# Performance work log

Hardware: AMD Instinct MI355X
Metric: run time of the kernel (lower is better)

Reference implementation:

```python
import jax, jax.numpy as jnp
import numpy as np

DIM = 2048
MLP_MULT = 4
NUM_EXPERTS = 8
EXPERT_INTER = MLP_MULT * DIM // NUM_EXPERTS  # 1024
B, S = 4, 2048


def setup_inputs() -> dict:
    key = jax.random.key(0)
    k1, k2, k3, k4 = jax.random.split(key, 4)
    x = jax.random.normal(k1, (B, S, DIM), dtype=jnp.float32)
    expert_ids = jax.random.randint(k2, (B, S), 0, NUM_EXPERTS, dtype=jnp.int64)
    # kaiming-uniform-ish scale for gate_up; down_proj random (zeros in orig init
    # would make output trivially zero, unhelpful for a correctness baseline)
    bound_gu = float(np.sqrt(1.0 / DIM))
    gate_up_proj = jax.random.uniform(k3, (NUM_EXPERTS, DIM, 2 * EXPERT_INTER),
                                      dtype=jnp.float32, minval=-bound_gu, maxval=bound_gu)
    bound_dn = float(np.sqrt(1.0 / EXPERT_INTER))
    down_proj = jax.random.uniform(k4, (NUM_EXPERTS, EXPERT_INTER, DIM),
                                   dtype=jnp.float32, minval=-bound_dn, maxval=bound_dn)
    return {"x": x, "expert_ids": expert_ids,
            "gate_up_proj": gate_up_proj, "down_proj": down_proj}


def reference(x, expert_ids, gate_up_proj, down_proj):
    Bb, Ss, D = x.shape
    E = gate_up_proj.shape[0]
    flat_x = x.reshape(-1, D)            # [T, D], T = B*S
    flat_ids = expert_ids.reshape(-1)    # [T]
    # Same math as the torch loop: full dense per-expert MLP, then mask.
    gu = jnp.einsum('td,edh->eth', flat_x, gate_up_proj)       # [E, T, 2I]
    g, u = jnp.split(gu, 2, axis=-1)                           # [E, T, I] each
    h = jax.nn.silu(g) * u                                     # [E, T, I]
    y = jnp.einsum('eti,eid->etd', h, down_proj)               # [E, T, D]
    mask = (flat_ids[None, :] == jnp.arange(E)[:, None])[..., None]  # [E, T, 1]
    out = jnp.sum(y * mask.astype(y.dtype), axis=0)            # [T, D]
    return out.reshape(Bb, Ss, D)
```

## Files before the change

kernel.cpp:

```cpp
#include <hip/hip_runtime.h>
#include <cstdint>
#include <cstddef>


typedef __attribute__((ext_vector_type(8))) _Float16 half8;
typedef __attribute__((ext_vector_type(4))) float floatx4;

#define AS_G __attribute__((address_space(1)))
#define AS_L __attribute__((address_space(3)))

__device__ __forceinline__ void async_cp16(void* lds, const void* g) {
  __builtin_amdgcn_global_load_lds((const AS_G uint32_t*)g, (AS_L uint32_t*)lds,
                                   16, 0, 0);
}

static constexpr int TTOK = 8192;
static constexpr int DIMK = 2048;
static constexpr int EI = 1024;
static constexpr int NE = 8;
static constexpr int PADT = 9216;
static constexpr int MAXTILES = 80;
static constexpr int NTILE_LAUNCH = 72;

__global__ __launch_bounds__(256) void k_route(const int* __restrict__ ids,
                                               int* __restrict__ perm,
                                               int* __restrict__ te,
                                               int* __restrict__ tr0,
                                               int* __restrict__ tnr,
                                               int* __restrict__ cur) {
  __shared__ int cnt[NE];
  __shared__ int sstart[NE];
  __shared__ int snpad[NE];
  __shared__ int stotal;
  int tid = threadIdx.x;
  if (tid < NE) cnt[tid] = 0;
  __syncthreads();
  for (int t = tid; t < TTOK; t += 256) atomicAdd(&cnt[ids[t]], 1);
  __syncthreads();
  if (tid == 0) {
    int pr = 0, nt = 0;
    for (int e = 0; e < NE; e++) {
      int n = cnt[e];
      sstart[e] = pr;
      cur[e] = pr;
      int padded = ((n + 127) >> 7) << 7;
      snpad[e] = padded - n;
      for (int j = 0; j < n; j += 128) {
        te[nt] = e; tr0[nt] = pr + j; tnr[nt] = min(128, n - j); nt++;
      }
      pr += padded;
    }
    stotal = pr;
    for (; nt < MAXTILES; nt++) { te[nt] = 0; tr0[nt] = 0; tnr[nt] = 0; }
  }
  __syncthreads();
  for (int e = 0; e < NE; e++) {
    int base = sstart[e] + cnt[e];
    for (int i = tid; i < snpad[e]; i += 256) perm[base + i] = 0;
  }
  for (int i = stotal + tid; i < PADT; i += 256) perm[i] = 0;
}

__global__ __launch_bounds__(256) void k_scatter(const int* __restrict__ ids,
                                                 int* __restrict__ cur,
                                                 int* __restrict__ perm) {
  __shared__ int bcnt[NE], bbase[NE], bloc[NE];
  int tid = threadIdx.x;
  int t = blockIdx.x * 256 + tid;
  if (tid < NE) { bcnt[tid] = 0; bloc[tid] = 0; }
  __syncthreads();
  int e = ids[t];
  atomicAdd(&bcnt[e], 1);
  __syncthreads();
  if (tid < NE && bcnt[tid] > 0) bbase[tid] = atomicAdd(&cur[tid], bcnt[tid]);
  __syncthreads();
  int off = atomicAdd(&bloc[e], 1);
  perm[bbase[e] + off] = t;
}

template <int K, int N>
__device__ __forceinline__ void transpose_tile(const float* __restrict__ src,
                                               _Float16* __restrict__ dst,
                                               float (*tile)[67], int e,
                                               int n0, int k0, int tid) {
  const float* s = src + (size_t)e * K * N;
  _Float16* d = dst + (size_t)e * N * K;
  int kk = tid >> 4;
  int nn = (tid & 15) * 4;
#pragma unroll
  for (int i = 0; i < 4; i++) {
    float4 v = *(const float4*)(s + (size_t)(k0 + kk + i * 16) * N + n0 + nn);
    tile[kk + i * 16][nn + 0] = v.x;
    tile[kk + i * 16][nn + 1] = v.y;
    tile[kk + i * 16][nn + 2] = v.z;
    tile[kk + i * 16][nn + 3] = v.w;
  }
  __syncthreads();
  int nrow = tid >> 3;
  int k8 = (tid & 7) * 8;
#pragma unroll
  for (int i = 0; i < 2; i++) {
    int n = nrow + i * 32;
    half8 o;
#pragma unroll
    for (int j = 0; j < 8; j++) o[j] = (_Float16)tile[k8 + j][n];
    *(half8*)(d + (size_t)(n0 + n) * K + k0 + k8) = o;
  }
}

__global__ __launch_bounds__(256) void k_prep(const float* __restrict__ gup,
                                              _Float16* __restrict__ wt1,
                                              const float* __restrict__ x,
                                              const int* __restrict__ perm,
                                              _Float16* __restrict__ xg) {
  __shared__ float tile[64][67];
  int b = blockIdx.x;
  int tid = threadIdx.x;
  if (b < 8192) {
    int e = b >> 10;
    int r = b & 1023;
    transpose_tile<DIMK, DIMK>(gup, wt1, tile, e, (r & 31) * 64, (r >> 5) * 64,
                               tid);
  } else {
    int row = b - 8192;
    int tok = perm[row];
    int c = tid * 8;
    const float* s = x + (size_t)tok * DIMK + c;
    float4 a = *(const float4*)s;
    float4 bb = *(const float4*)(s + 4);
    half8 o;
    o[0] = (_Float16)a.x; o[1] = (_Float16)a.y;
    o[2] = (_Float16)a.z; o[3] = (_Float16)a.w;
    o[4] = (_Float16)bb.x; o[5] = (_Float16)bb.y;
    o[6] = (_Float16)bb.z; o[7] = (_Float16)bb.w;
    *(half8*)(xg + (size_t)row * DIMK + c) = o;
  }
}

__global__ __launch_bounds__(256) void k_t2(const float* __restrict__ dwn,
                                            _Float16* __restrict__ wt2) {
  __shared__ float tile[64][67];
  transpose_tile<EI, DIMK>(dwn, wt2, tile, blockIdx.z, blockIdx.x * 64,
                           blockIdx.y * 64, threadIdx.x);
}

__global__ __launch_bounds__(256) void k_gateup(
    const _Float16* __restrict__ xg, const _Float16* __restrict__ wt1,
    const int* __restrict__ te, const int* __restrict__ tr0,
    const int* __restrict__ tnr, _Float16* __restrict__ hbuf) {
  int flat = blockIdx.y * 16 + blockIdx.x;
  int swz = (flat & 7) * (NTILE_LAUNCH * 16 / 8) + (flat >> 3);
  int tile = swz >> 4;
  int nr = tnr[tile];
  if (nr == 0) return;
  int e = te[tile], r0 = tr0[tile];
  int col = (swz & 15) * 64;
  int tid = threadIdx.x;

  __shared__ __align__(16) _Float16 As[2][128 * 64];
  __shared__ __align__(16) _Float16 Bg[2][64 * 64];
  __shared__ __align__(16) _Float16 Bu[2][64 * 64];

  int an = tid >> 2;
  int aq = (tid & 3) ^ ((tid >> 3) & 3);
  const _Float16* ap0 = xg + (size_t)(r0 + an) * DIMK + aq * 8;
  const _Float16* ap1 = ap0 + (size_t)64 * DIMK;
  const _Float16* bgp =
      wt1 + (size_t)e * DIMK * DIMK + (size_t)(col + an) * DIMK + aq * 8;
  const _Float16* bup = bgp + (size_t)EI * DIMK;

  int wave = tid >> 6, lane = tid & 63;
  int wm = (wave & 1) * 64, wn = (wave >> 1) * 32;
  int lm = lane & 15, lq = lane >> 4;
  int aoff[4], boff[2];
#pragma unroll
  for (int i = 0; i < 4; i++) {
    int r = wm + i * 16 + lm;
    aoff[i] = (r * 4 + (lq ^ ((r >> 1) & 3))) * 8;
  }
#pragma unroll
  for (int j = 0; j < 2; j++) {
    int n = wn + j * 16 + lm;
    boff[j] = (n * 4 + (lq ^ ((n >> 1) & 3))) * 8;
  }

  floatx4 accg[4][2], accu[4][2];
#pragma unroll
  for (int i = 0; i < 4; i++)
#pragma unroll
    for (int j = 0; j < 2; j++) {
      accg[i][j] = (floatx4)0.0f;
      accu[i][j] = (floatx4)0.0f;
    }

  auto stage = [&](int p, int k0) {
    _Float16* a = As[p] + (size_t)tid * 8;
    _Float16* g = Bg[p] + (size_t)tid * 8;
    _Float16* u = Bu[p] + (size_t)tid * 8;
    async_cp16(a, ap0 + k0);
    async_cp16(a + 2048, ap1 + k0);
    async_cp16(g, bgp + k0);
    async_cp16(u, bup + k0);
    async_cp16(a + 4096, ap0 + k0 + 32);
    async_cp16(a + 6144, ap1 + k0 + 32);
    async_cp16(g + 2048, bgp + k0 + 32);
    async_cp16(u + 2048, bup + k0 + 32);
  };

  stage(0, 0);
  __syncthreads();

  int p = 0;
  for (int k0 = 0; k0 < DIMK; k0 += 64, p ^= 1) {
    if (k0 + 64 < DIMK) stage(p ^ 1, k0 + 64);
#pragma unroll
    for (int s = 0; s < 2; s++) {
      const _Float16* Ab = As[p] + s * 4096;
      const _Float16* Bgb = Bg[p] + s * 2048;
      const _Float16* Bub = Bu[p] + s * 2048;
      half8 af[4], bgf[2], buf_[2];
#pragma unroll
      for (int i = 0; i < 4; i++) af[i] = *(const half8*)(Ab + aoff[i]);
#pragma unroll
      for (int j = 0; j < 2; j++) {
        bgf[j] = *(const half8*)(Bgb + boff[j]);
        buf_[j] = *(const half8*)(Bub + boff[j]);
      }
#pragma unroll
      for (int i = 0; i < 4; i++)
#pragma unroll
        for (int j = 0; j < 2; j++) {
          accg[i][j] = __builtin_amdgcn_mfma_f32_16x16x32_f16(
              af[i], bgf[j], accg[i][j], 0, 0, 0);
          accu[i][j] = __builtin_amdgcn_mfma_f32_16x16x32_f16(
              af[i], buf_[j], accu[i][j], 0, 0, 0);
        }
    }
    __syncthreads();
  }

#pragma unroll
  for (int i = 0; i < 4; i++) {
    int rbase = wm + i * 16 + lq * 4;
#pragma unroll
    for (int j = 0; j < 2; j++) {
      int c = col + wn + j * 16 + lm;
#pragma unroll
      for (int rr = 0; rr < 4; rr++) {
        float g = accg[i][j][rr];
        float u = accu[i][j][rr];
        float h = g / (1.0f + __expf(-g)) * u;
        hbuf[(size_t)(r0 + rbase + rr) * EI + c] = (_Float16)h;
      }
    }
  }
}

__global__ __launch_bounds__(256) void k_down(
    const _Float16* __restrict__ hbuf, const _Float16* __restrict__ wt2,
    const int* __restrict__ perm, const int* __restrict__ te,
    const int* __restrict__ tr0, const int* __restrict__ tnr,
    float* __restrict__ out) {
  int flat = blockIdx.y * 16 + blockIdx.x;
  int swz = (flat & 7) * (NTILE_LAUNCH * 16 / 8) + (flat >> 3);
  int tile = swz >> 4;
  int nr = tnr[tile];
  if (nr == 0) return;
  int e = te[tile], r0 = tr0[tile];
  int col = (swz & 15) * 128;
  int tid = threadIdx.x;

  __shared__ __align__(16) _Float16 As[2][128 * 64];
  __shared__ __align__(16) _Float16 Bs[2][128 * 64];

  int an = tid >> 2;
  int aq = (tid & 3) ^ ((tid >> 3) & 3);
  const _Float16* ap0 = hbuf + (size_t)(r0 + an) * EI + aq * 8;
  const _Float16* ap1 = ap0 + (size_t)64 * EI;
  const _Float16* wte = wt2 + (size_t)e * DIMK * EI;
  const _Float16* bp0 = wte + (size_t)(col + an) * EI + aq * 8;
  const _Float16* bp1 = bp0 + (size_t)64 * EI;

  int wave = tid >> 6, lane = tid & 63;
  int wm = (wave & 1) * 64, wn = (wave >> 1) * 64;
  int lm = lane & 15, lq = lane >> 4;
  int aoff[4], boff[4];
#pragma unroll
  for (int i = 0; i < 4; i++) {
    int r = wm + i * 16 + lm;
    aoff[i] = (r * 4 + (lq ^ ((r >> 1) & 3))) * 8;
    int n = wn + i * 16 + lm;
    boff[i] = (n * 4 + (lq ^ ((n >> 1) & 3))) * 8;
  }

  floatx4 acc[4][4];
#pragma unroll
  for (int i = 0; i < 4; i++)
#pragma unroll
    for (int j = 0; j < 4; j++) acc[i][j] = (floatx4)0.0f;

  auto stage = [&](int p, int k0) {
    _Float16* a = As[p] + (size_t)tid * 8;
    _Float16* b = Bs[p] + (size_t)tid * 8;
    async_cp16(a, ap0 + k0);
    async_cp16(a + 2048, ap1 + k0);
    async_cp16(b, bp0 + k0);
    async_cp16(b + 2048, bp1 + k0);
    async_cp16(a + 4096, ap0 + k0 + 32);
    async_cp16(a + 6144, ap1 + k0 + 32);
    async_cp16(b + 4096, bp0 + k0 + 32);
    async_cp16(b + 6144, bp1 + k0 + 32);
  };

  stage(0, 0);
  __syncthreads();

  int p = 0;
  for (int k0 = 0; k0 < EI; k0 += 64, p ^= 1) {
    if (k0 + 64 < EI) stage(p ^ 1, k0 + 64);
#pragma unroll
    for (int s = 0; s < 2; s++) {
      const _Float16* Ab = As[p] + s * 4096;
      const _Float16* Bb = Bs[p] + s * 4096;
      half8 af[4], bf[4];
#pragma unroll
      for (int i = 0; i < 4; i++) {
        af[i] = *(const half8*)(Ab + aoff[i]);
        bf[i] = *(const half8*)(Bb + boff[i]);
      }
#pragma unroll
      for (int i = 0; i < 4; i++)
#pragma unroll
        for (int j = 0; j < 4; j++)
          acc[i][j] = __builtin_amdgcn_mfma_f32_16x16x32_f16(af[i], bf[j],
                                                             acc[i][j], 0, 0, 0);
    }
    __syncthreads();
  }

#pragma unroll
  for (int i = 0; i < 4; i++) {
    int rbase = wm + i * 16 + lq * 4;
#pragma unroll
    for (int rr = 0; rr < 4; rr++) {
      int r = rbase + rr;
      if (r < nr) {
        int tok = perm[r0 + r];
        float* orow = out + (size_t)tok * DIMK + col;
#pragma unroll
        for (int j = 0; j < 4; j++) orow[wn + j * 16 + lm] = acc[i][j][rr];
      }
    }
  }
}

extern "C" void kernel_launch(void* const* d_in, const int* in_sizes, int n_in,
                              void* d_out, int out_size, void* d_ws,
                              size_t ws_size, hipStream_t stream) {
  const float* x = (const float*)d_in[0];
  const int* ids = (const int*)d_in[1];
  const float* gup = (const float*)d_in[2];
  const float* dwn = (const float*)d_in[3];
  float* out = (float*)d_out;
  char* ws = (char*)d_ws;

  int* perm = (int*)ws;
  int* te = (int*)(ws + 36864);
  int* tr0 = (int*)(ws + 36864 + 512);
  int* tnr = (int*)(ws + 36864 + 1024);
  int* cur = (int*)(ws + 36864 + 1536);
  _Float16* wt1 = (_Float16*)(ws + 65536);
  _Float16* hbuf = (_Float16*)(ws + 65536 + 67108864);
  _Float16* xg = (_Float16*)(ws + 65536 + 67108864 + 18874368);
  _Float16* wt2 = wt1;

  k_route<<<dim3(1), dim3(256), 0, stream>>>(ids, perm, te, tr0, tnr, cur);
  k_scatter<<<dim3(32), dim3(256), 0, stream>>>(ids, cur, perm);
  k_prep<<<dim3(8192 + PADT), dim3(256), 0, stream>>>(gup, wt1, x, perm, xg);
  k_gateup<<<dim3(16, NTILE_LAUNCH), dim3(256), 0, stream>>>(
      xg, wt1, te, tr0, tnr, hbuf);
  k_t2<<<dim3(32, 16, 8), dim3(256), 0, stream>>>(dwn, wt2);
  k_down<<<dim3(16, NTILE_LAUNCH), dim3(256), 0, stream>>>(
      hbuf, wt2, perm, te, tr0, tnr, out);
}
```

Before: 500.1 us.

## Deepen GEMM pipelines to four-stage K32 ring with vmcnt-based waits

Both grouped GEMM kernels switch from a double-buffered K=64 loop with __syncthreads to a four-buffer ring of K=32 slices. Three stages stay in flight, and each step waits only for the oldest slice with explicit s_waitcnt vmcnt and a bare s_barrier. MFMA blocks are wrapped in sched_barrier and s_setprio to raise wave priority during matrix math. The intent is to hide global-load latency better and cut the cost of the full sync. In exchange there is one barrier per 32-wide K step instead of per 64. Correctness now depends on hand-tuned vmcnt counts.

```diff
diff --git a/kernel.cpp b/kernel.cpp
--- a/kernel.cpp
+++ b/kernel.cpp
@@ -157,9 +157,9 @@
   int col = (swz & 15) * 64;
   int tid = threadIdx.x;
 
-  __shared__ __align__(16) _Float16 As[2][128 * 64];
-  __shared__ __align__(16) _Float16 Bg[2][64 * 64];
-  __shared__ __align__(16) _Float16 Bu[2][64 * 64];
+  __shared__ __align__(16) _Float16 As[4][4096];
+  __shared__ __align__(16) _Float16 Bg[4][2048];
+  __shared__ __align__(16) _Float16 Bu[4][2048];
 
   int an = tid >> 2;
   int aq = (tid & 3) ^ ((tid >> 3) & 3);
@@ -194,50 +194,59 @@
     }
 
   auto stage = [&](int p, int k0) {
-    _Float16* a = As[p] + (size_t)tid * 8;
-    _Float16* g = Bg[p] + (size_t)tid * 8;
-    _Float16* u = Bu[p] + (size_t)tid * 8;
-    async_cp16(a, ap0 + k0);
-    async_cp16(a + 2048, ap1 + k0);
-    async_cp16(g, bgp + k0);
-    async_cp16(u, bup + k0);
-    async_cp16(a + 4096, ap0 + k0 + 32);
-    async_cp16(a + 6144, ap1 + k0 + 32);
-    async_cp16(g + 2048, bgp + k0 + 32);
-    async_cp16(u + 2048, bup + k0 + 32);
+    async_cp16(&As[p][(size_t)tid * 8], ap0 + k0);
+    async_cp16(&As[p][2048 + (size_t)tid * 8], ap1 + k0);
+    async_cp16(&Bg[p][(size_t)tid * 8], bgp + k0);
+    async_cp16(&Bu[p][(size_t)tid * 8], bup + k0);
   };
 
+  auto compute = [&](int b) {
+    half8 af[4], bgf[2], buf_[2];
+#pragma unroll
+    for (int i = 0; i < 4; i++) af[i] = *(const half8*)(&As[b][0] + aoff[i]);
+#pragma unroll
+    for (int j = 0; j < 2; j++) {
+      bgf[j] = *(const half8*)(&Bg[b][0] + boff[j]);
+      buf_[j] = *(const half8*)(&Bu[b][0] + boff[j]);
+    }
+    asm volatile("s_waitcnt lgkmcnt(0)" ::: "memory");
+    __builtin_amdgcn_sched_barrier(0);
+    __builtin_amdgcn_s_setprio(1);
+#pragma unroll
+    for (int i = 0; i < 4; i++)
+#pragma unroll
+      for (int j = 0; j < 2; j++) {
+        accg[i][j] = __builtin_amdgcn_mfma_f32_16x16x32_f16(
+            af[i], bgf[j], accg[i][j], 0, 0, 0);
+        accu[i][j] = __builtin_amdgcn_mfma_f32_16x16x32_f16(
+            af[i], buf_[j], accu[i][j], 0, 0, 0);
+      }
+    __builtin_amdgcn_s_setprio(0);
+  };
+
   stage(0, 0);
-  __syncthreads();
-
-  int p = 0;
-  for (int k0 = 0; k0 < DIMK; k0 += 64, p ^= 1) {
-    if (k0 + 64 < DIMK) stage(p ^ 1, k0 + 64);
-#pragma unroll
-    for (int s = 0; s < 2; s++) {
-      const _Float16* Ab = As[p] + s * 4096;
-      const _Float16* Bgb = Bg[p] + s * 2048;
-      const _Float16* Bub = Bu[p] + s * 2048;
-      half8 af[4], bgf[2], buf_[2];
-#pragma unroll
-      for (int i = 0; i < 4; i++) af[i] = *(const half8*)(Ab + aoff[i]);
-#pragma unroll
-      for (int j = 0; j < 2; j++) {
-        bgf[j] = *(const half8*)(Bgb + boff[j]);
-        buf_[j] = *(const half8*)(Bub + boff[j]);
-      }
-#pragma unroll
-      for (int i = 0; i < 4; i++)
-#pragma unroll
-        for (int j = 0; j < 2; j++) {
-          accg[i][j] = __builtin_amdgcn_mfma_f32_16x16x32_f16(
-              af[i], bgf[j], accg[i][j], 0, 0, 0);
-          accu[i][j] = __builtin_amdgcn_mfma_f32_16x16x32_f16(
-              af[i], buf_[j], accu[i][j], 0, 0, 0);
-        }
-    }
-    __syncthreads();
-  }
+  stage(1, 32);
+  stage(2, 64);
+
+  int b = 0;
+  for (int k = 0; k < 61; ++k) {
+    asm volatile("s_waitcnt vmcnt(8)" ::: "memory");
+    __builtin_amdgcn_s_barrier();
+    stage((b + 3) & 3, (k + 3) * 32);
+    compute(b);
+    b = (b + 1) & 3;
+  }
+  asm volatile("s_waitcnt vmcnt(8)" ::: "memory");
+  __builtin_amdgcn_s_barrier();
+  compute(b);
+  b = (b + 1) & 3;
+  asm volatile("s_waitcnt vmcnt(4)" ::: "memory");
+  __builtin_amdgcn_s_barrier();
+  compute(b);
+  b = (b + 1) & 3;
+  asm volatile("s_waitcnt vmcnt(0)" ::: "memory");
+  __builtin_amdgcn_s_barrier();
+  compute(b);
 
 #pragma unroll
   for (int i = 0; i < 4; i++) {
@@ -270,8 +279,8 @@
   int col = (swz & 15) * 128;
   int tid = threadIdx.x;
 
-  __shared__ __align__(16) _Float16 As[2][128 * 64];
-  __shared__ __align__(16) _Float16 Bs[2][128 * 64];
+  __shared__ __align__(16) _Float16 As[4][4096];
+  __shared__ __align__(16) _Float16 Bs[4][4096];
 
   int an = tid >> 2;
   int aq = (tid & 3) ^ ((tid >> 3) & 3);
@@ -300,43 +309,54 @@
     for (int j = 0; j < 4; j++) acc[i][j] = (floatx4)0.0f;
 
   auto stage = [&](int p, int k0) {
-    _Float16* a = As[p] + (size_t)tid * 8;
-    _Float16* b = Bs[p] + (size_t)tid * 8;
-    async_cp16(a, ap0 + k0);
-    async_cp16(a + 2048, ap1 + k0);
-    async_cp16(b, bp0 + k0);
-    async_cp16(b + 2048, bp1 + k0);
-    async_cp16(a + 4096, ap0 + k0 + 32);
-    async_cp16(a + 6144, ap1 + k0 + 32);
-    async_cp16(b + 4096, bp0 + k0 + 32);
-    async_cp16(b + 6144, bp1 + k0 + 32);
+    async_cp16(&As[p][(size_t)tid * 8], ap0 + k0);
+    async_cp16(&As[p][2048 + (size_t)tid * 8], ap1 + k0);
+    async_cp16(&Bs[p][(size_t)tid * 8], bp0 + k0);
+    async_cp16(&Bs[p][2048 + (size_t)tid * 8], bp1 + k0);
   };
 
+  auto compute = [&](int b) {
+    half8 af[4], bf[4];
+#pragma unroll
+    for (int i = 0; i < 4; i++) {
+      af[i] = *(const half8*)(&As[b][0] + aoff[i]);
+      bf[i] = *(const half8*)(&Bs[b][0] + boff[i]);
+    }
+    asm volatile("s_waitcnt lgkmcnt(0)" ::: "memory");
+    __builtin_amdgcn_sched_barrier(0);
+    __builtin_amdgcn_s_setprio(1);
+#pragma unroll
+    for (int i = 0; i < 4; i++)
+#pragma unroll
+      for (int j = 0; j < 4; j++)
+        acc[i][j] = __builtin_amdgcn_mfma_f32_16x16x32_f16(af[i], bf[j],
+                                                           acc[i][j], 0, 0, 0);
+    __builtin_amdgcn_s_setprio(0);
+  };
+
   stage(0, 0);
-  __syncthreads();
-
-  int p = 0;
-  for (int k0 = 0; k0 < EI; k0 += 64, p ^= 1) {
-    if (k0 + 64 < EI) stage(p ^ 1, k0 + 64);
-#pragma unroll
-    for (int s = 0; s < 2; s++) {
-      const _Float16* Ab = As[p] + s * 4096;
-      const _Float16* Bb = Bs[p] + s * 4096;
-      half8 af[4], bf[4];
-#pragma unroll
-      for (int i = 0; i < 4; i++) {
-        af[i] = *(const half8*)(Ab + aoff[i]);
-        bf[i] = *(const half8*)(Bb + boff[i]);
-      }
-#pragma unroll
-      for (int i = 0; i < 4; i++)
-#pragma unroll
-        for (int j = 0; j < 4; j++)
-          acc[i][j] = __builtin_amdgcn_mfma_f32_16x16x32_f16(af[i], bf[j],
-                                                             acc[i][j], 0, 0, 0);
-    }
-    __syncthreads();
-  }
+  stage(1, 32);
+  stage(2, 64);
+
+  int b = 0;
+  for (int k = 0; k < 29; ++k) {
+    asm volatile("s_waitcnt vmcnt(8)" ::: "memory");
+    __builtin_amdgcn_s_barrier();
+    stage((b + 3) & 3, (k + 3) * 32);
+    compute(b);
+    b = (b + 1) & 3;
+  }
+  asm volatile("s_waitcnt vmcnt(8)" ::: "memory");
+  __builtin_amdgcn_s_barrier();
+  compute(b);
+  b = (b + 1) & 3;
+  asm volatile("s_waitcnt vmcnt(4)" ::: "memory");
+  __builtin_amdgcn_s_barrier();
+  compute(b);
+  b = (b + 1) & 3;
+  asm volatile("s_waitcnt vmcnt(0)" ::: "memory");
+  __builtin_amdgcn_s_barrier();
+  compute(b);
 
 #pragma unroll
   for (int i = 0; i < 4; i++) {
```

Result: slower. 528.3 us (+5.6%).

## Use 256-row expert tiles with 512-thread blocks in both GEMMs

Applied to the files above, without the earlier changes.

Routing now emits tiles of 256 rows per expert, with a 128- or 256-row tail tile, and records each tile's size. The gate/up and down GEMM kernels become 512-thread blocks computing 256x256 output tiles (gate and up fused into one B tile) with 8x4 MFMA accumulators per wave. This raises arithmetic intensity and reuse of weight and activation loads, and cuts the number of launched tiles. The cost is heavier register use at one block per CU, fewer blocks overall (up to 320) which may leave CUs idle, and more padded rows in tail tiles.

```diff
diff --git a/kernel.cpp b/kernel.cpp
--- a/kernel.cpp
+++ b/kernel.cpp
@@ -19,14 +19,15 @@
 static constexpr int EI = 1024;
 static constexpr int NE = 8;
 static constexpr int PADT = 9216;
-static constexpr int MAXTILES = 80;
-static constexpr int NTILE_LAUNCH = 72;
+static constexpr int MAXTILES = 40;
+static constexpr int NT_LAUNCH = 40;
 
 __global__ __launch_bounds__(256) void k_route(const int* __restrict__ ids,
                                                int* __restrict__ perm,
                                                int* __restrict__ te,
                                                int* __restrict__ tr0,
                                                int* __restrict__ tnr,
+                                               int* __restrict__ tts,
                                                int* __restrict__ cur) {
   __shared__ int cnt[NE];
   __shared__ int sstart[NE];
@@ -43,15 +44,21 @@
       int n = cnt[e];
       sstart[e] = pr;
       cur[e] = pr;
-      int padded = ((n + 127) >> 7) << 7;
+      int full = n >> 8, rem = n & 255;
+      for (int j = 0; j < full; j++) {
+        te[nt] = e; tr0[nt] = pr + j * 256; tnr[nt] = 256; tts[nt] = 256; nt++;
+      }
+      int padded = full * 256;
+      if (rem) {
+        int tsz = (rem <= 128) ? 128 : 256;
+        te[nt] = e; tr0[nt] = pr + padded; tnr[nt] = rem; tts[nt] = tsz; nt++;
+        padded += tsz;
+      }
       snpad[e] = padded - n;
-      for (int j = 0; j < n; j += 128) {
-        te[nt] = e; tr0[nt] = pr + j; tnr[nt] = min(128, n - j); nt++;
-      }
       pr += padded;
     }
     stotal = pr;
-    for (; nt < MAXTILES; nt++) { te[nt] = 0; tr0[nt] = 0; tnr[nt] = 0; }
+    for (; nt < MAXTILES; nt++) { te[nt] = 0; tr0[nt] = 0; tnr[nt] = 0; tts[nt] = 128; }
   }
   __syncthreads();
   for (int e = 0; e < NE; e++) {
@@ -144,211 +151,216 @@
                            blockIdx.y * 64, threadIdx.x);
 }
 
-__global__ __launch_bounds__(256) void k_gateup(
+__global__ __launch_bounds__(512, 1) void k_gu(
     const _Float16* __restrict__ xg, const _Float16* __restrict__ wt1,
     const int* __restrict__ te, const int* __restrict__ tr0,
-    const int* __restrict__ tnr, _Float16* __restrict__ hbuf) {
-  int flat = blockIdx.y * 16 + blockIdx.x;
-  int swz = (flat & 7) * (NTILE_LAUNCH * 16 / 8) + (flat >> 3);
-  int tile = swz >> 4;
+    const int* __restrict__ tnr, const int* __restrict__ tts,
+    _Float16* __restrict__ hbuf) {
+  int flat = blockIdx.y * 8 + blockIdx.x;
+  int swz = (flat & 7) * NT_LAUNCH + (flat >> 3);
+  int tile = swz >> 3, cb = swz & 7;
   int nr = tnr[tile];
   if (nr == 0) return;
-  int e = te[tile], r0 = tr0[tile];
-  int col = (swz & 15) * 64;
-  int tid = threadIdx.x;
-
-  __shared__ __align__(16) _Float16 As[2][128 * 64];
-  __shared__ __align__(16) _Float16 Bg[2][64 * 64];
-  __shared__ __align__(16) _Float16 Bu[2][64 * 64];
-
-  int an = tid >> 2;
-  int aq = (tid & 3) ^ ((tid >> 3) & 3);
-  const _Float16* ap0 = xg + (size_t)(r0 + an) * DIMK + aq * 8;
-  const _Float16* ap1 = ap0 + (size_t)64 * DIMK;
-  const _Float16* bgp =
-      wt1 + (size_t)e * DIMK * DIMK + (size_t)(col + an) * DIMK + aq * 8;
-  const _Float16* bup = bgp + (size_t)EI * DIMK;
-
-  int wave = tid >> 6, lane = tid & 63;
-  int wm = (wave & 1) * 64, wn = (wave >> 1) * 32;
-  int lm = lane & 15, lq = lane >> 4;
-  int aoff[4], boff[2];
-#pragma unroll
-  for (int i = 0; i < 4; i++) {
-    int r = wm + i * 16 + lm;
+  int e = te[tile], r0 = tr0[tile], tsz = tts[tile];
+  int tid = threadIdx.x;
+
+  __shared__ __align__(16) _Float16 As[2][16384];
+  __shared__ __align__(16) _Float16 Bs[2][16384];
+
+  int arow = tid >> 2;
+  int slot = tid & 3;
+  int cg = (slot ^ ((arow >> 1) & 3)) * 8;
+  int arow1 = (tsz == 256) ? 128 + arow : arow;
+  const _Float16* apA = xg + (size_t)(r0 + arow) * DIMK;
+  const _Float16* apB = xg + (size_t)(r0 + arow1) * DIMK;
+  const _Float16* wte = wt1 + (size_t)e * DIMK * DIMK;
+  const _Float16* bpG = wte + (size_t)(cb * 128 + arow) * DIMK;
+  const _Float16* bpU = wte + (size_t)(EI + cb * 128 + arow) * DIMK;
+
+  auto stage = [&](int p, int k0) {
+#pragma unroll
+    for (int s = 0; s < 2; s++) {
+      int go = k0 + s * 32 + cg;
+      _Float16* al = &As[p][s * 8192 + tid * 8];
+      _Float16* bl = &Bs[p][s * 8192 + tid * 8];
+      async_cp16(al, apA + go);
+      async_cp16(al + 4096, apB + go);
+      async_cp16(bl, bpG + go);
+      async_cp16(bl + 4096, bpU + go);
+    }
+  };
+
+  int wave = tid >> 6;
+  int wr = wave >> 2, wc = wave & 3;
+  int lane = tid & 63, lm = lane & 15, lq = lane >> 4;
+  int aoff[8], boff[4];
+#pragma unroll
+  for (int i = 0; i < 8; i++) {
+    int r = wr * 128 + i * 16 + lm;
     aoff[i] = (r * 4 + (lq ^ ((r >> 1) & 3))) * 8;
   }
 #pragma unroll
-  for (int j = 0; j < 2; j++) {
-    int n = wn + j * 16 + lm;
-    boff[j] = (n * 4 + (lq ^ ((n >> 1) & 3))) * 8;
-  }
-
-  floatx4 accg[4][2], accu[4][2];
-#pragma unroll
-  for (int i = 0; i < 4; i++)
+  for (int j = 0; j < 4; j++) {
+    int br = (j < 2) ? (wc * 32 + j * 16 + lm)
+                     : (128 + wc * 32 + (j - 2) * 16 + lm);
+    boff[j] = (br * 4 + (lq ^ ((br >> 1) & 3))) * 8;
+  }
+
+  floatx4 acc[8][4];
+#pragma unroll
+  for (int i = 0; i < 8; i++)
+#pragma unroll
+    for (int j = 0; j < 4; j++) acc[i][j] = (floatx4)0.0f;
+
+  auto compute = [&](int p) {
+#pragma unroll
+    for (int s = 0; s < 2; s++) {
+      const _Float16* Ab = &As[p][s * 8192];
+      const _Float16* Bb = &Bs[p][s * 8192];
+      half8 af[8], bf[4];
+#pragma unroll
+      for (int i = 0; i < 8; i++) af[i] = *(const half8*)(Ab + aoff[i]);
+#pragma unroll
+      for (int j = 0; j < 4; j++) bf[j] = *(const half8*)(Bb + boff[j]);
+#pragma unroll
+      for (int i = 0; i < 8; i++)
+#pragma unroll
+        for (int j = 0; j < 4; j++)
+          acc[i][j] = __builtin_amdgcn_mfma_f32_16x16x32_f16(af[i], bf[j],
+                                                             acc[i][j], 0, 0, 0);
+    }
+  };
+
+  stage(0, 0);
+  __syncthreads();
+  for (int k0 = 0; k0 < DIMK; k0 += 128) {
+    if (k0 + 64 < DIMK) stage(1, k0 + 64);
+    compute(0);
+    __syncthreads();
+    if (k0 + 128 < DIMK) stage(0, k0 + 128);
+    compute(1);
+    __syncthreads();
+  }
+
+#pragma unroll
+  for (int i = 0; i < 8; i++) {
+    int rl0 = wr * 128 + i * 16;
+    if (rl0 >= tsz) continue;
 #pragma unroll
     for (int j = 0; j < 2; j++) {
-      accg[i][j] = (floatx4)0.0f;
-      accu[i][j] = (floatx4)0.0f;
-    }
-
-  auto stage = [&](int p, int k0) {
-    _Float16* a = As[p] + (size_t)tid * 8;
-    _Float16* g = Bg[p] + (size_t)tid * 8;
-    _Float16* u = Bu[p] + (size_t)tid * 8;
-    async_cp16(a, ap0 + k0);
-    async_cp16(a + 2048, ap1 + k0);
-    async_cp16(g, bgp + k0);
-    async_cp16(u, bup + k0);
-    async_cp16(a + 4096, ap0 + k0 + 32);
-    async_cp16(a + 6144, ap1 + k0 + 32);
-    async_cp16(g + 2048, bgp + k0 + 32);
-    async_cp16(u + 2048, bup + k0 + 32);
-  };
-
-  stage(0, 0);
-  __syncthreads();
-
-  int p = 0;
-  for (int k0 = 0; k0 < DIMK; k0 += 64, p ^= 1) {
-    if (k0 + 64 < DIMK) stage(p ^ 1, k0 + 64);
-#pragma unroll
-    for (int s = 0; s < 2; s++) {
-      const _Float16* Ab = As[p] + s * 4096;
-      const _Float16* Bgb = Bg[p] + s * 2048;
-      const _Float16* Bub = Bu[p] + s * 2048;
-      half8 af[4], bgf[2], buf_[2];
-#pragma unroll
-      for (int i = 0; i < 4; i++) af[i] = *(const half8*)(Ab + aoff[i]);
-#pragma unroll
-      for (int j = 0; j < 2; j++) {
-        bgf[j] = *(const half8*)(Bgb + boff[j]);
-        buf_[j] = *(const half8*)(Bub + boff[j]);
+      int c = cb * 128 + wc * 32 + j * 16 + lm;
+#pragma unroll
+      for (int rr = 0; rr < 4; rr++) {
+        float g = acc[i][j][rr];
+        float u = acc[i][j + 2][rr];
+        float h = g / (1.0f + __expf(-g)) * u;
+        hbuf[(size_t)(r0 + rl0 + lq * 4 + rr) * EI + c] = (_Float16)h;
       }
-#pragma unroll
-      for (int i = 0; i < 4; i++)
-#pragma unroll
-        for (int j = 0; j < 2; j++) {
-          accg[i][j] = __builtin_amdgcn_mfma_f32_16x16x32_f16(
-              af[i], bgf[j], accg[i][j], 0, 0, 0);
-          accu[i][j] = __builtin_amdgcn_mfma_f32_16x16x32_f16(
-              af[i], buf_[j], accu[i][j], 0, 0, 0);
-        }
-    }
-    __syncthreads();
-  }
-
-#pragma unroll
-  for (int i = 0; i < 4; i++) {
-    int rbase = wm + i * 16 + lq * 4;
-#pragma unroll
-    for (int j = 0; j < 2; j++) {
-      int c = col + wn + j * 16 + lm;
-#pragma unroll
-      for (int rr = 0; rr < 4; rr++) {
-        float g = accg[i][j][rr];
-        float u = accu[i][j][rr];
-        float h = g / (1.0f + __expf(-g)) * u;
-        hbuf[(size_t)(r0 + rbase + rr) * EI + c] = (_Float16)h;
-      }
-    }
-  }
-}
-
-__global__ __launch_bounds__(256) void k_down(
+    }
+  }
+}
+
+__global__ __launch_bounds__(512, 1) void k_dn(
     const _Float16* __restrict__ hbuf, const _Float16* __restrict__ wt2,
     const int* __restrict__ perm, const int* __restrict__ te,
     const int* __restrict__ tr0, const int* __restrict__ tnr,
-    float* __restrict__ out) {
-  int flat = blockIdx.y * 16 + blockIdx.x;
-  int swz = (flat & 7) * (NTILE_LAUNCH * 16 / 8) + (flat >> 3);
-  int tile = swz >> 4;
+    const int* __restrict__ tts, float* __restrict__ out) {
+  int flat = blockIdx.y * 8 + blockIdx.x;
+  int swz = (flat & 7) * NT_LAUNCH + (flat >> 3);
+  int tile = swz >> 3, cb = swz & 7;
   int nr = tnr[tile];
   if (nr == 0) return;
-  int e = te[tile], r0 = tr0[tile];
-  int col = (swz & 15) * 128;
-  int tid = threadIdx.x;
-
-  __shared__ __align__(16) _Float16 As[2][128 * 64];
-  __shared__ __align__(16) _Float16 Bs[2][128 * 64];
-
-  int an = tid >> 2;
-  int aq = (tid & 3) ^ ((tid >> 3) & 3);
-  const _Float16* ap0 = hbuf + (size_t)(r0 + an) * EI + aq * 8;
-  const _Float16* ap1 = ap0 + (size_t)64 * EI;
+  int e = te[tile], r0 = tr0[tile], tsz = tts[tile];
+  int tid = threadIdx.x;
+
+  __shared__ __align__(16) _Float16 As[2][16384];
+  __shared__ __align__(16) _Float16 Bs[2][16384];
+
+  int arow = tid >> 2;
+  int slot = tid & 3;
+  int cg = (slot ^ ((arow >> 1) & 3)) * 8;
+  int arow1 = (tsz == 256) ? 128 + arow : arow;
+  const _Float16* apA = hbuf + (size_t)(r0 + arow) * EI;
+  const _Float16* apB = hbuf + (size_t)(r0 + arow1) * EI;
   const _Float16* wte = wt2 + (size_t)e * DIMK * EI;
-  const _Float16* bp0 = wte + (size_t)(col + an) * EI + aq * 8;
-  const _Float16* bp1 = bp0 + (size_t)64 * EI;
-
-  int wave = tid >> 6, lane = tid & 63;
-  int wm = (wave & 1) * 64, wn = (wave >> 1) * 64;
-  int lm = lane & 15, lq = lane >> 4;
-  int aoff[4], boff[4];
-#pragma unroll
-  for (int i = 0; i < 4; i++) {
-    int r = wm + i * 16 + lm;
+  const _Float16* bp0 = wte + (size_t)(cb * 256 + arow) * EI;
+  const _Float16* bp1 = wte + (size_t)(cb * 256 + 128 + arow) * EI;
+
+  auto stage = [&](int p, int k0) {
+#pragma unroll
+    for (int s = 0; s < 2; s++) {
+      int go = k0 + s * 32 + cg;
+      _Float16* al = &As[p][s * 8192 + tid * 8];
+      _Float16* bl = &Bs[p][s * 8192 + tid * 8];
+      async_cp16(al, apA + go);
+      async_cp16(al + 4096, apB + go);
+      async_cp16(bl, bp0 + go);
+      async_cp16(bl + 4096, bp1 + go);
+    }
+  };
+
+  int wave = tid >> 6;
+  int wr = wave >> 2, wc = wave & 3;
+  int lane = tid & 63, lm = lane & 15, lq = lane >> 4;
+  int aoff[8], boff[4];
+#pragma unroll
+  for (int i = 0; i < 8; i++) {
+    int r = wr * 128 + i * 16 + lm;
     aoff[i] = (r * 4 + (lq ^ ((r >> 1) & 3))) * 8;
-    int n = wn + i * 16 + lm;
-    boff[i] = (n * 4 + (lq ^ ((n >> 1) & 3))) * 8;
-  }
-
-  floatx4 acc[4][4];
-#pragma unroll
-  for (int i = 0; i < 4; i++)
+  }
+#pragma unroll
+  for (int j = 0; j < 4; j++) {
+    int br = wc * 64 + j * 16 + lm;
+    boff[j] = (br * 4 + (lq ^ ((br >> 1) & 3))) * 8;
+  }
+
+  floatx4 acc[8][4];
+#pragma unroll
+  for (int i = 0; i < 8; i++)
 #pragma unroll
     for (int j = 0; j < 4; j++) acc[i][j] = (floatx4)0.0f;
 
-  auto stage = [&](int p, int k0) {
-    _Float16* a = As[p] + (size_t)tid * 8;
-    _Float16* b = Bs[p] + (size_t)tid * 8;
-    async_cp16(a, ap0 + k0);
-    async_cp16(a + 2048, ap1 + k0);
-    async_cp16(b, bp0 + k0);
-    async_cp16(b + 2048, bp1 + k0);
-    async_cp16(a + 4096, ap0 + k0 + 32);
-    async_cp16(a + 6144, ap1 + k0 + 32);
-    async_cp16(b + 4096, bp0 + k0 + 32);
-    async_cp16(b + 6144, bp1 + k0 + 32);
-  };
-
-  stage(0, 0);
-  __syncthreads();
-
-  int p = 0;
-  for (int k0 = 0; k0 < EI; k0 += 64, p ^= 1) {
-    if (k0 + 64 < EI) stage(p ^ 1, k0 + 64);
+  auto compute = [&](int p) {
 #pragma unroll
     for (int s = 0; s < 2; s++) {
-      const _Float16* Ab = As[p] + s * 4096;
-      const _Float16* Bb = Bs[p] + s * 4096;
-      half8 af[4], bf[4];
-#pragma unroll
-      for (int i = 0; i < 4; i++) {
-        af[i] = *(const half8*)(Ab + aoff[i]);
-        bf[i] = *(const half8*)(Bb + boff[i]);
-      }
-#pragma unroll
-      for (int i = 0; i < 4; i++)
+      const _Float16* Ab = &As[p][s * 8192];
+      const _Float16* Bb = &Bs[p][s * 8192];
+      half8 af[8], bf[4];
+#pragma unroll
+      for (int i = 0; i < 8; i++) af[i] = *(const half8*)(Ab + aoff[i]);
+#pragma unroll
+      for (int j = 0; j < 4; j++) bf[j] = *(const half8*)(Bb + boff[j]);
+#pragma unroll
+      for (int i = 0; i < 8; i++)
 #pragma unroll
         for (int j = 0; j < 4; j++)
           acc[i][j] = __builtin_amdgcn_mfma_f32_16x16x32_f16(af[i], bf[j],
                                                              acc[i][j], 0, 0, 0);
     }
+  };
+
+  stage(0, 0);
+  __syncthreads();
+  for (int k0 = 0; k0 < EI; k0 += 128) {
+    if (k0 + 64 < EI) stage(1, k0 + 64);
+    compute(0);
     __syncthreads();
-  }
-
-#pragma unroll
-  for (int i = 0; i < 4; i++) {
-    int rbase = wm + i * 16 + lq * 4;
+    if (k0 + 128 < EI) stage(0, k0 + 128);
+    compute(1);
+    __syncthreads();
+  }
+
+#pragma unroll
+  for (int i = 0; i < 8; i++) {
+    int rl0 = wr * 128 + i * 16;
 #pragma unroll
     for (int rr = 0; rr < 4; rr++) {
-      int r = rbase + rr;
+      int r = rl0 + lq * 4 + rr;
       if (r < nr) {
         int tok = perm[r0 + r];
-        float* orow = out + (size_t)tok * DIMK + col;
-#pragma unroll
-        for (int j = 0; j < 4; j++) orow[wn + j * 16 + lm] = acc[i][j][rr];
+        float* orow = out + (size_t)tok * DIMK + cb * 256;
+#pragma unroll
+        for (int j = 0; j < 4; j++) orow[wc * 64 + j * 16 + lm] = acc[i][j][rr];
       }
     }
   }
@@ -366,20 +378,21 @@
 
   int* perm = (int*)ws;
   int* te = (int*)(ws + 36864);
-  int* tr0 = (int*)(ws + 36864 + 512);
-  int* tnr = (int*)(ws + 36864 + 1024);
-  int* cur = (int*)(ws + 36864 + 1536);
+  int* tr0 = (int*)(ws + 37376);
+  int* tnr = (int*)(ws + 37888);
+  int* tts = (int*)(ws + 38400);
+  int* cur = (int*)(ws + 38912);
   _Float16* wt1 = (_Float16*)(ws + 65536);
   _Float16* hbuf = (_Float16*)(ws + 65536 + 67108864);
   _Float16* xg = (_Float16*)(ws + 65536 + 67108864 + 18874368);
   _Float16* wt2 = wt1;
 
-  k_route<<<dim3(1), dim3(256), 0, stream>>>(ids, perm, te, tr0, tnr, cur);
+  k_route<<<dim3(1), dim3(256), 0, stream>>>(ids, perm, te, tr0, tnr, tts, cur);
   k_scatter<<<dim3(32), dim3(256), 0, stream>>>(ids, cur, perm);
   k_prep<<<dim3(8192 + PADT), dim3(256), 0, stream>>>(gup, wt1, x, perm, xg);
-  k_gateup<<<dim3(16, NTILE_LAUNCH), dim3(256), 0, stream>>>(
-      xg, wt1, te, tr0, tnr, hbuf);
+  k_gu<<<dim3(8, NT_LAUNCH), dim3(512), 0, stream>>>(
+      xg, wt1, te, tr0, tnr, tts, hbuf);
   k_t2<<<dim3(32, 16, 8), dim3(256), 0, stream>>>(dwn, wt2);
-  k_down<<<dim3(16, NTILE_LAUNCH), dim3(256), 0, stream>>>(
-      hbuf, wt2, perm, te, tr0, tnr, out);
-}
+  k_dn<<<dim3(8, NT_LAUNCH), dim3(512), 0, stream>>>(
+      hbuf, wt2, perm, te, tr0, tnr, tts, out);
+}
```

New measurement: 507.1 us. About the same (+1.4%).
